# Performance work log

Hardware: AMD Instinct MI355X
Metric: run time of the kernel (lower is better)

## Reference

```python
import jax, jax.numpy as jnp
from jax import lax
import numpy as np

B, OBS, PRED, F, H = 2048, 20, 30, 16, 1024


def _lstm_layer(x, Wih, Whh, bih, bhh):
    # x: [T, B, in]; PyTorch gate order i, f, g, o; zero initial state
    Bb = x.shape[1]
    Hh = Whh.shape[1]
    def step(carry, xt):
        h, c = carry
        g = xt @ Wih.T + h @ Whh.T + bih + bhh
        i, f, gg, o = jnp.split(g, 4, axis=-1)
        c = jax.nn.sigmoid(f) * c + jax.nn.sigmoid(i) * jnp.tanh(gg)
        h = jax.nn.sigmoid(o) * jnp.tanh(c)
        return (h, c), h
    z = jnp.zeros((Bb, Hh), x.dtype)
    _, hs = lax.scan(step, (z, z), x)
    return hs  # [T, B, H]


def _lstm2(x, Wih0, Whh0, bih0, bhh0, Wih1, Whh1, bih1, bhh1):
    return _lstm_layer(_lstm_layer(x, Wih0, Whh0, bih0, bhh0), Wih1, Whh1, bih1, bhh1)


def setup_inputs() -> dict:
    key = jax.random.key(0)
    ks = jax.random.split(key, 32)
    s = 0.05
    def w(k, shape):
        return jax.random.normal(k, shape, dtype=jnp.float32) * s
    d = {
        'x_in': jax.random.normal(ks[0], (B, OBS, F), dtype=jnp.float32),
        'y': jax.random.normal(ks[1], (B, PRED, F), dtype=jnp.float32),
        'v_in': jax.random.normal(ks[2], (B, OBS, F), dtype=jnp.float32),
        'sx': jnp.ones((1,), jnp.float32),
        'sv': jnp.ones((1,), jnp.float32),
    }
    i = 3
    for p in ['v', 'a']:
        d[p + 'Wih0'] = w(ks[i], (4 * H, F)); i += 1
        d[p + 'Whh0'] = w(ks[i], (4 * H, H)); i += 1
        d[p + 'bih0'] = w(ks[i], (4 * H,)); i += 1
        d[p + 'bhh0'] = w(ks[i], (4 * H,)); i += 1
        d[p + 'Wih1'] = w(ks[i], (4 * H, H)); i += 1
        d[p + 'Whh1'] = w(ks[i], (4 * H, H)); i += 1
        d[p + 'bih1'] = w(ks[i], (4 * H,)); i += 1
        d[p + 'bhh1'] = w(ks[i], (4 * H,)); i += 1
        d[p + 'Wl'] = w(ks[i], (F, H)); i += 1
        d[p + 'bl'] = w(ks[i], (F,)); i += 1
    return d


def reference(x_in, y, v_in, sx, sv,
              vWih0, vWhh0, vbih0, vbhh0, vWih1, vWhh1, vbih1, vbhh1, vWl, vbl,
              aWih0, aWhh0, abih0, abhh0, aWih1, aWhh1, abih1, abhh1, aWl, abl):
    # last observed position, scaled: [1, B, F]
    x = jnp.transpose(x_in, (1, 0, 2))[-1:] * sx
    yT = sx * jnp.transpose(y, (1, 0, 2))  # [PRED, B, F]
    v_seq = jnp.transpose(v_in, (1, 0, 2))  # [OBS, B, F]
    a_seq = v_seq[1:] - v_seq[:-1]          # [OBS-1, B, F]

    vh = _lstm2(v_seq, vWih0, vWhh0, vbih0, vbhh0, vWih1, vWhh1, vbih1, vbhh1)
    v = sv * jnp.tanh(vh[-1:] @ vWl.T + vbl)  # [1, B, F]

    ah = _lstm2(a_seq, aWih0, aWhh0, abih0, abhh0, aWih1, aWhh1, abih1, abhh1)
    a = jnp.tanh(ah @ aWl.T + abl)[-1:]       # [1, B, F] (unscaled, fed back)

    v = v + sv * a
    x = x + v

    def body(carry, _):
        a, v, x = carry
        # NOTE: faithful to source -- LSTM state resets to zero each step
        ah = _lstm2(a, aWih0, aWhh0, abih0, abhh0, aWih1, aWhh1, abih1, abhh1)
        a = jnp.tanh(ah @ aWl.T + abl)
        v = v + sv * a
        x = x + v
        return (a, v, x), x[0]

    _, xs = lax.scan(body, (a, v, x), None, length=PRED - 1)  # xs: [PRED-1, B, F]
    out = jnp.concatenate([x, xs], axis=0)  # [PRED, B, F]
    return (out, yT)
```

## Files before the change

kernel.cpp:

```cpp
#include <hip/hip_runtime.h>


#define B_    2048
#define OBS_  20
#define PRED_ 30
#define F_    16
#define H_    1024
#define GN_   4096

typedef _Float16 f16;
typedef _Float16 f16x8 __attribute__((ext_vector_type(8)));
typedef _Float16 f16x4 __attribute__((ext_vector_type(4)));
typedef float    f32x4 __attribute__((ext_vector_type(4)));

__device__ __forceinline__ float fast_sigmoid(float x) {
  return 1.0f / (1.0f + __expf(-x));
}
__device__ __forceinline__ float fast_tanh(float x) {
  float ax = fabsf(x);
  float e  = __expf(-2.0f * ax);
  float r  = (1.0f - e) / (1.0f + e);
  return copysignf(r, x);
}

__device__ __forceinline__ void stageA(f16* dst, const f16* Asrc, int b0, int k0, int tid) {
#pragma unroll
  for (int cc = 0; cc < 2; ++cc) {
    int o  = cc * 4096 + tid * 16;
    int rr = o >> 6;
    int sp = (o >> 4) & 3;
    int sl = sp ^ ((rr >> 1) & 3);
    const f16* gp = Asrc + (size_t)(b0 + rr) * H_ + k0 + sl * 8;
    __builtin_amdgcn_global_load_lds(
        (const __attribute__((address_space(1))) void*)gp,
        (__attribute__((address_space(3))) void*)((char*)dst + o), 16, 0, 0);
  }
}
__device__ __forceinline__ void stageB(f16* dst, const f16* Wsrc, int j0, int k0, int tid) {
#pragma unroll
  for (int cc = 0; cc < 2; ++cc) {
    int o  = cc * 4096 + tid * 16;
    int rr = o >> 6;
    int sp = (o >> 4) & 3;
    int sl = sp ^ ((rr >> 1) & 3);
    int row = (rr >> 5) * H_ + j0 + (rr & 31);
    const f16* gp = Wsrc + (size_t)row * H_ + k0 + sl * 8;
    __builtin_amdgcn_global_load_lds(
        (const __attribute__((address_space(1))) void*)gp,
        (__attribute__((address_space(3))) void*)((char*)dst + o), 16, 0, 0);
  }
}

__device__ __forceinline__ void acc_init(f32x4 (&acc)[4][4], const float* bias, int jcol) {
#pragma unroll
  for (int g = 0; g < 4; ++g) {
    float bv = bias[g * H_ + jcol];
#pragma unroll
    for (int m = 0; m < 4; ++m) acc[m][g] = (f32x4){bv, bv, bv, bv};
  }
}

__device__ __forceinline__ void run_k16(f32x4 (&acc)[4][4], const f16* A16, const f16* W16,
    int b0, int j0, int wr, int wc, int lcol, int lkq)
{
  f16x8 za = {0, 0, 0, 0, 0, 0, 0, 0};
  f16x8 af[4], bf[4];
#pragma unroll
  for (int m = 0; m < 4; ++m) {
    if (lkq < 2) {
      int row = b0 + wr * 64 + m * 16 + lcol;
      af[m] = *(const f16x8*)(A16 + (size_t)row * 16 + lkq * 8);
    } else af[m] = za;
  }
#pragma unroll
  for (int g = 0; g < 4; ++g) {
    if (lkq < 2) {
      int row = g * H_ + j0 + wc * 16 + lcol;
      bf[g] = *(const f16x8*)(W16 + (size_t)row * 16 + lkq * 8);
    } else bf[g] = za;
  }
#pragma unroll
  for (int m = 0; m < 4; ++m)
#pragma unroll
    for (int g = 0; g < 4; ++g)
      acc[m][g] = __builtin_amdgcn_mfma_f32_16x16x32_f16(af[m], bf[g], acc[m][g], 0, 0, 0);
}

__device__ __forceinline__ void kstep_mfma(f32x4 (&acc)[4][4], const f16* lA, const f16* lB,
    int wr, int wc, int lcol, int lkq)
{
  f16x8 av[4], bw[4];
#pragma unroll
  for (int m = 0; m < 4; ++m) {
    int ar = wr * 64 + m * 16 + lcol;
    int sa = lkq ^ ((ar >> 1) & 3);
    av[m] = *(const f16x8*)&lA[ar * 32 + sa * 8];
  }
#pragma unroll
  for (int g = 0; g < 4; ++g) {
    int br = g * 32 + wc * 16 + lcol;
    int sb = lkq ^ ((br >> 1) & 3);
    bw[g] = *(const f16x8*)&lB[br * 32 + sb * 8];
  }
#pragma unroll
  for (int m = 0; m < 4; ++m)
#pragma unroll
    for (int g = 0; g < 4; ++g)
      acc[m][g] = __builtin_amdgcn_mfma_f32_16x16x32_f16(av[m], bw[g], acc[m][g], 0, 0, 0);
}

__device__ __forceinline__ void run_kloop_rt(f32x4 (&acc)[4][4],
    f16 (*lA)[4096], f16 (*lB)[4096],
    const f16* A0, const f16* W0, const f16* A1, const f16* W1,
    int NT, int NTSW,
    int b0, int j0, int tid, int wr, int wc, int lcol, int lkq)
{
  int cur = 0;
  for (int t = 0; t < NT; ++t) {
    if (t + 1 < NT) {
      int tn = t + 1;
      const f16* As = (tn >= NTSW) ? A1 : A0;
      const f16* Ws = (tn >= NTSW) ? W1 : W0;
      int k0 = (tn & 31) * 32;
      stageA(lA[cur ^ 1], As, b0, k0, tid);
      stageB(lB[cur ^ 1], Ws, j0, k0, tid);
      asm volatile("s_waitcnt vmcnt(4)\n\ts_barrier" ::: "memory");
    } else {
      asm volatile("s_waitcnt vmcnt(0)\n\ts_barrier" ::: "memory");
    }
    kstep_mfma(acc, lA[cur], lB[cur], wr, wc, lcol, lkq);
    asm volatile("s_waitcnt lgkmcnt(0)\n\ts_barrier" ::: "memory");
    cur ^= 1;
  }
}

__device__ __forceinline__ void lstm_epi_g(f32x4 (&acc)[4][4], const float* cin, float* cout,
    f16* hout, int b0, int jcol, int wr, int lkq, int hasc, int writec)
{
#pragma unroll
  for (int m = 0; m < 4; ++m) {
    int brow0 = b0 + wr * 64 + m * 16 + lkq * 4;
#pragma unroll
    for (int r = 0; r < 4; ++r) {
      size_t bi = (size_t)(brow0 + r) * H_ + jcol;
      float gi = acc[m][0][r], gf = acc[m][1][r], gg = acc[m][2][r], go = acc[m][3][r];
      float cold = hasc ? cin[bi] : 0.0f;
      float cn = fast_sigmoid(gf) * cold + fast_sigmoid(gi) * fast_tanh(gg);
      float hv = fast_sigmoid(go) * fast_tanh(cn);
      if (writec) cout[bi] = cn;
      hout[bi] = (f16)hv;
    }
  }
}

struct StepArgs {
  const f16* A16; const f16* W16v; const f16* W16a;
  const f16* A0;  const f16* W0v;  const f16* W0a;
  const f16* A1;  const f16* W1v;  const f16* W1a;
  const float* bv; const float* ba;
  const float* cin; float* cout; f16* hout;
  int k16, nt, hasc, writec;
};

__device__ __forceinline__ void lstm_body(const StepArgs& p, f16 (*lA)[4096], f16 (*lB)[4096], int bi)
{
  const int tid = threadIdx.x, lane = tid & 63;
  const int wv = tid >> 6, wr = wv >> 1, wc = wv & 1;
  const int bm = bi >> 5, bn = bi & 31;
  const int b0 = bm * 128, j0 = bn * 32;
  const int ch = bm >> 4;
  const int lcol = lane & 15, lkq = lane >> 4;
  const int jcol = j0 + wc * 16 + lcol;

  const f16* W16 = ch ? p.W16a : p.W16v;
  const f16* W0  = ch ? p.W0a  : p.W0v;
  const f16* W1  = ch ? p.W1a  : p.W1v;
  const float* bias = ch ? p.ba : p.bv;

  if (p.nt) { stageA(lA[0], p.A0, b0, 0, tid); stageB(lB[0], W0, j0, 0, tid); }
  f32x4 acc[4][4];
  acc_init(acc, bias, jcol);
  if (p.k16) run_k16(acc, p.A16, W16, b0, j0, wr, wc, lcol, lkq);
  if (p.nt)
    run_kloop_rt(acc, lA, lB, p.A0, W0, p.A1, W1, p.nt, 32, b0, j0, tid, wr, wc, lcol, lkq);
  lstm_epi_g(acc, p.cin, p.cout, p.hout, b0, jcol, wr, lkq, p.hasc, p.writec);
}

__global__ __launch_bounds__(256, 4)
void obs_pair(StepArgs q, StepArgs r, int split)
{
  __shared__ f16 lA[2][4096];
  __shared__ f16 lB[2][4096];
  int blk = blockIdx.x;
  if (blk < split) lstm_body(q, lA, lB, blk);
  else             lstm_body(r, lA, lB, blk - split);
}

__global__ __launch_bounds__(256, 4)
void scan_l1(const f16* __restrict__ h0, const f16* __restrict__ Wih1,
             const float* __restrict__ bias1, const float* __restrict__ Wl,
             float* __restrict__ ppart)
{
  __shared__ f16 lA[2][4096];
  __shared__ f16 lB[2][4096];
  __shared__ f16 hl[128 * 40];
  const int tid = threadIdx.x, lane = tid & 63;
  const int wv = tid >> 6, wr = wv >> 1, wc = wv & 1;
  const int bm = blockIdx.x >> 5, bn = blockIdx.x & 31;
  const int b0 = bm * 128, j0 = bn * 32;
  const int lcol = lane & 15, lkq = lane >> 4;
  const int jcol = j0 + wc * 16 + lcol;

  stageA(lA[0], h0, b0, 0, tid);
  stageB(lB[0], Wih1, j0, 0, tid);
  f32x4 acc[4][4];
  acc_init(acc, bias1, jcol);
  run_kloop_rt(acc, lA, lB, h0, Wih1, nullptr, nullptr, 32, 32, b0, j0, tid, wr, wc, lcol, lkq);

  int jl = wc * 16 + lcol;
#pragma unroll
  for (int m = 0; m < 4; ++m) {
#pragma unroll
    for (int r = 0; r < 4; ++r) {
      int row = wr * 64 + m * 16 + lkq * 4 + r;
      float gi = acc[m][0][r], gf = acc[m][1][r], gg = acc[m][2][r], go = acc[m][3][r];
      (void)gf;
      float cn = fast_sigmoid(gi) * fast_tanh(gg);
      float hv = fast_sigmoid(go) * fast_tanh(cn);
      hl[row * 40 + jl] = (f16)hv;
    }
  }
  __syncthreads();

  const float* wrow = Wl + (size_t)lcol * H_ + j0 + lkq * 8;
  float4 w0 = *(const float4*)wrow, w1 = *(const float4*)(wrow + 4);
  f16x8 bf = {(f16)w0.x, (f16)w0.y, (f16)w0.z, (f16)w0.w,
              (f16)w1.x, (f16)w1.y, (f16)w1.z, (f16)w1.w};
#pragma unroll
  for (int mt = 0; mt < 2; ++mt) {
    int arow = wv * 32 + mt * 16 + lcol;
    f16x8 af = *(const f16x8*)&hl[arow * 40 + lkq * 8];
    f32x4 pc = {0, 0, 0, 0};
    pc = __builtin_amdgcn_mfma_f32_16x16x32_f16(af, bf, pc, 0, 0, 0);
#pragma unroll
    for (int r = 0; r < 4; ++r) {
      int row = b0 + wv * 32 + mt * 16 + lkq * 4 + r;
      ppart[(size_t)row * 512 + bn * 16 + lcol] = pc[r];
    }
  }
}

template<int FIRST, int LAST>
__global__ __launch_bounds__(256, 4)
void scan_l0(const float* __restrict__ ppart, const f16* __restrict__ a16f,
             const float* __restrict__ bl, const float* __restrict__ sv,
             float* __restrict__ v_buf, float* __restrict__ x_buf,
             float* __restrict__ out_t,
             const float* __restrict__ bias0, const f16* __restrict__ Wih0,
             f16* __restrict__ h0out)
{
  __shared__ f16 a_lds[128 * 16];
  const int tid = threadIdx.x;
  const int bm = LAST ? (int)blockIdx.x : (int)(blockIdx.x >> 5);
  const int bn = LAST ? 0 : (int)(blockIdx.x & 31);
  const int b0 = bm * 128;

  const int ebase = tid * 8;
  const int erow  = ebase >> 4;
  const int ef0   = ebase & 15;
  float av[8];
  if (FIRST) {
    f16x8 a8 = *(const f16x8*)&a16f[(size_t)(b0 + erow) * 16 + ef0];
#pragma unroll
    for (int e = 0; e < 8; ++e) av[e] = (float)a8[e];
  } else {
    f32x4 s0 = {0, 0, 0, 0}, s1 = {0, 0, 0, 0};
    const float* pp = ppart + (size_t)(b0 + erow) * 512 + ef0;
#pragma unroll
    for (int sN = 0; sN < 32; ++sN) {
      s0 += *(const f32x4*)(pp + sN * 16);
      s1 += *(const f32x4*)(pp + sN * 16 + 4);
    }
#pragma unroll
    for (int e = 0; e < 4; ++e) av[e] = fast_tanh(s0[e] + bl[ef0 + e]);
#pragma unroll
    for (int e = 0; e < 4; ++e) av[4 + e] = fast_tanh(s1[e] + bl[ef0 + 4 + e]);
    if (bn == 0) {
      float svv = sv[0];
#pragma unroll
      for (int e = 0; e < 8; ++e) {
        int idx = (b0 + erow) * F_ + ef0 + e;
        float v = v_buf[idx] + svv * av[e];
        v_buf[idx] = v;
        float x = x_buf[idx] + v;
        x_buf[idx] = x;
        out_t[idx] = x;
      }
    }
  }

  if (!LAST) {
    f16x8 a8;
#pragma unroll
    for (int e = 0; e < 8; ++e) a8[e] = (f16)av[e];
    *(f16x8*)&a_lds[ebase] = a8;
    __syncthreads();

    const int lane = tid & 63;
    const int wv = tid >> 6, wr = wv >> 1, wc = wv & 1;
    const int lcol = lane & 15, lkq = lane >> 4;
    const int j0 = bn * 32, jcol = j0 + wc * 16 + lcol;
    f32x4 acc[4][4];
    acc_init(acc, bias0, jcol);
    f16x8 za = {0, 0, 0, 0, 0, 0, 0, 0};
    f16x8 af[4], bf[4];
#pragma unroll
    for (int m = 0; m < 4; ++m) {
      if (lkq < 2) {
        int arow = wr * 64 + m * 16 + lcol;
        af[m] = *(const f16x8*)&a_lds[arow * 16 + lkq * 8];
      } else af[m] = za;
    }
#pragma unroll
    for (int g = 0; g < 4; ++g) {
      if (lkq < 2) {
        int brow = g * H_ + j0 + wc * 16 + lcol;
        bf[g] = *(const f16x8*)(Wih0 + (size_t)brow * 16 + lkq * 8);
      } else bf[g] = za;
    }
#pragma unroll
    for (int m = 0; m < 4; ++m)
#pragma unroll
      for (int g = 0; g < 4; ++g)
        acc[m][g] = __builtin_amdgcn_mfma_f32_16x16x32_f16(af[m], bf[g], acc[m][g], 0, 0, 0);
    lstm_epi_g(acc, nullptr, nullptr, h0out, b0, jcol, wr, lkq, 0, 0);
  }
}

template<int MODE>
__global__ __launch_bounds__(256)
void proj_update(const f16* __restrict__ h1, const float* __restrict__ Wl,
                 const float* __restrict__ bl, const float* __restrict__ sv,
                 float* __restrict__ v_buf, float* __restrict__ x_buf,
                 float* __restrict__ out_t, f16* __restrict__ a16)
{
  __shared__ f16 lh[16 * 1024];
  const int b0r = blockIdx.x * 16;
  const int tid = threadIdx.x;
#pragma unroll
  for (int c = 0; c < 8; ++c) {
    int o = c * 256 + tid;
    *(f16x8*)&lh[o * 8] = *(const f16x8*)&h1[(size_t)b0r * 1024 + o * 8];
  }
  __syncthreads();
  const int br = tid >> 4;
  const int f  = tid & 15;
  float s0 = 0, s1 = 0, s2 = 0, s3 = 0;
  const float4* wp = (const float4*)(Wl + (size_t)f * 1024);
#pragma unroll 4
  for (int k8 = 0; k8 < 128; ++k8) {
    f16x8 hv = *(const f16x8*)&lh[br * 1024 + k8 * 8];
    float4 w0 = wp[k8 * 2], w1 = wp[k8 * 2 + 1];
    s0 += (float)hv[0] * w0.x + (float)hv[4] * w1.x;
    s1 += (float)hv[1] * w0.y + (float)hv[5] * w1.y;
    s2 += (float)hv[2] * w0.z + (float)hv[6] * w1.z;
    s3 += (float)hv[3] * w0.w + (float)hv[7] * w1.w;
  }
  float t = fast_tanh(bl[f] + ((s0 + s1) + (s2 + s3)));
  int idx = (b0r + br) * F_ + f;
  if (MODE == 0) {
    v_buf[idx] = sv[0] * t;
  } else {
    float v = v_buf[idx] + sv[0] * t;
    v_buf[idx] = v;
    float x = x_buf[idx] + v;
    x_buf[idx] = x;
    out_t[idx] = x;
    a16[idx] = (f16)t;
  }
}

__global__ void prep_kernel(const float* __restrict__ x_in, const float* __restrict__ y,
                            const float* __restrict__ v_in, const float* __restrict__ sx,
                            float* __restrict__ out, float* __restrict__ x_buf,
                            f16* __restrict__ m16)
{
  const float s = sx[0];
  int gid = blockIdx.x * blockDim.x + threadIdx.x;
  int gs  = gridDim.x * blockDim.x;
  for (int i = gid; i < B_ * OBS_ * F_; i += gs) {
    int b = i / (OBS_ * F_);
    int rem = i - b * (OBS_ * F_);
    int t = rem >> 4;
    int f = rem & 15;
    float v = v_in[i];
    m16[((size_t)t * 4096 + b) * F_ + f] = (f16)v;
    if (t < OBS_ - 1)
      m16[((size_t)t * 4096 + 2048 + b) * F_ + f] = (f16)(v_in[i + F_] - v);
  }
  for (int i = gid; i < PRED_ * B_ * F_; i += gs) {
    int t = i / (B_ * F_);
    int rem = i - t * (B_ * F_);
    int b = rem >> 4;
    int f = rem & 15;
    out[PRED_ * B_ * F_ + i] = s * y[(b * PRED_ + t) * F_ + f];
  }
  for (int i = gid; i < B_ * F_; i += gs) {
    int b = i >> 4;
    int f = i & 15;
    x_buf[i] = s * x_in[(b * OBS_ + (OBS_ - 1)) * F_ + f];
  }
}

struct ConvArgs {
  const float* src[8];
  f16*         dst[8];
  int          n[8];
  const float* b1[4];
  const float* b2[4];
  float*       bd[4];
};

__global__ void convw(ConvArgs a)
{
  int gid = blockIdx.x * blockDim.x + threadIdx.x;
  int gs  = gridDim.x * blockDim.x;
#pragma unroll
  for (int s = 0; s < 8; ++s) {
    int n4 = a.n[s] >> 2;
    for (int i = gid; i < n4; i += gs) {
      float4 v = ((const float4*)a.src[s])[i];
      f16x4 d = {(f16)v.x, (f16)v.y, (f16)v.z, (f16)v.w};
      ((f16x4*)a.dst[s])[i] = d;
    }
  }
#pragma unroll
  for (int s = 0; s < 4; ++s) {
    for (int i = gid; i < GN_; i += gs) a.bd[s][i] = a.b1[s][i] + a.b2[s][i];
  }
}

extern "C" void kernel_launch(void* const* d_in, const int* in_sizes, int n_in,
                              void* d_out, int out_size, void* d_ws, size_t ws_size,
                              hipStream_t stream)
{
  (void)in_sizes; (void)n_in; (void)out_size; (void)ws_size;

  const float* x_in  = (const float*)d_in[0];
  const float* y     = (const float*)d_in[1];
  const float* v_in  = (const float*)d_in[2];
  const float* sx    = (const float*)d_in[3];
  const float* sv    = (const float*)d_in[4];
  const float* vWih0 = (const float*)d_in[5];
  const float* vWhh0 = (const float*)d_in[6];
  const float* vbih0 = (const float*)d_in[7];
  const float* vbhh0 = (const float*)d_in[8];
  const float* vWih1 = (const float*)d_in[9];
  const float* vWhh1 = (const float*)d_in[10];
  const float* vbih1 = (const float*)d_in[11];
  const float* vbhh1 = (const float*)d_in[12];
  const float* vWl   = (const float*)d_in[13];
  const float* vbl   = (const float*)d_in[14];
  const float* aWih0 = (const float*)d_in[15];
  const float* aWhh0 = (const float*)d_in[16];
  const float* abih0 = (const float*)d_in[17];
  const float* abhh0 = (const float*)d_in[18];
  const float* aWih1 = (const float*)d_in[19];
  const float* aWhh1 = (const float*)d_in[20];
  const float* abih1 = (const float*)d_in[21];
  const float* abhh1 = (const float*)d_in[22];
  const float* aWl   = (const float*)d_in[23];
  const float* abl   = (const float*)d_in[24];
  float* out = (float*)d_out;

  char* ws = (char*)d_ws;
  size_t off = 0;
  auto alloc = [&](size_t bytes) {
    char* p = ws + off;
    off += (bytes + 255) & ~(size_t)255;
    return p;
  };
  f16* vWih0f = (f16*)alloc((size_t)GN_ * F_ * 2);
  f16* vWhh0f = (f16*)alloc((size_t)GN_ * H_ * 2);
  f16* vWih1f = (f16*)alloc((size_t)GN_ * H_ * 2);
  f16* vWhh1f = (f16*)alloc((size_t)GN_ * H_ * 2);
  f16* aWih0f = (f16*)alloc((size_t)GN_ * F_ * 2);
  f16* aWhh0f = (f16*)alloc((size_t)GN_ * H_ * 2);
  f16* aWih1f = (f16*)alloc((size_t)GN_ * H_ * 2);
  f16* aWhh1f = (f16*)alloc((size_t)GN_ * H_ * 2);
  float* vb0 = (float*)alloc(GN_ * 4);
  float* vb1 = (float*)alloc(GN_ * 4);
  float* ab0 = (float*)alloc(GN_ * 4);
  float* ab1 = (float*)alloc(GN_ * 4);
  f16* m16 = (f16*)alloc((size_t)OBS_ * 4096 * F_ * 2);
  f16* h0a = (f16*)alloc((size_t)4096 * H_ * 2);
  f16* h0b = (f16*)alloc((size_t)4096 * H_ * 2);
  f16* h1a = (f16*)alloc((size_t)4096 * H_ * 2);
  f16* h1b = (f16*)alloc((size_t)4096 * H_ * 2);
  float* c0 = (float*)alloc((size_t)4096 * H_ * 4);
  float* c1 = (float*)alloc((size_t)4096 * H_ * 4);
  f16* a16   = (f16*)alloc((size_t)B_ * F_ * 2);
  float* v_buf = (float*)alloc((size_t)B_ * F_ * 4);
  float* x_buf = (float*)alloc((size_t)B_ * F_ * 4);
  float* ppart = (float*)alloc((size_t)B_ * 32 * F_ * 4);

  ConvArgs ca;
  ca.src[0] = vWih0; ca.dst[0] = vWih0f; ca.n[0] = GN_ * F_;
  ca.src[1] = vWhh0; ca.dst[1] = vWhh0f; ca.n[1] = GN_ * H_;
  ca.src[2] = vWih1; ca.dst[2] = vWih1f; ca.n[2] = GN_ * H_;
  ca.src[3] = vWhh1; ca.dst[3] = vWhh1f; ca.n[3] = GN_ * H_;
  ca.src[4] = aWih0; ca.dst[4] = aWih0f; ca.n[4] = GN_ * F_;
  ca.src[5] = aWhh0; ca.dst[5] = aWhh0f; ca.n[5] = GN_ * H_;
  ca.src[6] = aWih1; ca.dst[6] = aWih1f; ca.n[6] = GN_ * H_;
  ca.src[7] = aWhh1; ca.dst[7] = aWhh1f; ca.n[7] = GN_ * H_;
  ca.b1[0] = vbih0; ca.b2[0] = vbhh0; ca.bd[0] = vb0;
  ca.b1[1] = vbih1; ca.b2[1] = vbhh1; ca.bd[1] = vb1;
  ca.b1[2] = abih0; ca.b2[2] = abhh0; ca.bd[2] = ab0;
  ca.b1[3] = abih1; ca.b2[3] = abhh1; ca.bd[3] = ab1;
  convw<<<1024, 256, 0, stream>>>(ca);
  prep_kernel<<<1024, 256, 0, stream>>>(x_in, y, v_in, sx, out, x_buf, m16);

  auto h0buf = [&](int t) { return (t & 1) ? h0b : h0a; };
  auto h1buf = [&](int t) { return (t & 1) ? h1b : h1a; };
  StepArgs dummy{};

  {
    StepArgs q{};
    q.A16 = m16; q.W16v = vWih0f; q.W16a = aWih0f;
    q.bv = vb0; q.ba = ab0;
    q.cout = c0; q.hout = h0buf(0);
    q.k16 = 1; q.nt = 0; q.hasc = 0; q.writec = 1;
    obs_pair<<<1024, 256, 0, stream>>>(q, dummy, 1024);
  }

  for (int t = 1; t < OBS_; ++t) {
    int u = t - 1;
    StepArgs q{};
    q.A16 = m16 + (size_t)t * 4096 * F_;
    q.W16v = vWih0f; q.W16a = aWih0f;
    q.A0 = h0buf(t - 1); q.W0v = vWhh0f; q.W0a = aWhh0f;
    q.bv = vb0; q.ba = ab0;
    q.cin = c0; q.cout = c0; q.hout = h0buf(t);
    q.k16 = 1; q.nt = 32; q.hasc = 1; q.writec = 1;

    StepArgs r{};
    r.A0 = h0buf(u); r.W0v = vWih1f; r.W0a = aWih1f;
    r.A1 = (u > 0) ? h1buf(u - 1) : nullptr;
    r.W1v = vWhh1f; r.W1a = aWhh1f;
    r.bv = vb1; r.ba = ab1;
    r.cin = c1; r.cout = c1; r.hout = h1buf(u);
    r.k16 = 0; r.nt = (u > 0) ? 64 : 32; r.hasc = (u > 0); r.writec = 1;

    int split = (t == OBS_ - 1) ? 512 : 1024;
    int grid  = (t == OBS_ - 1) ? 1536 : 2048;
    obs_pair<<<grid, 256, 0, stream>>>(q, r, split);
  }

  {
    StepArgs r{};
    r.A0 = h0buf(19); r.W0v = vWih1f; r.W0a = aWih1f;
    r.A1 = h1buf(18); r.W1v = vWhh1f; r.W1a = aWhh1f;
    r.bv = vb1; r.ba = ab1;
    r.cin = c1; r.cout = c1; r.hout = h1buf(19);
    r.k16 = 0; r.nt = 64; r.hasc = 1; r.writec = 1;
    obs_pair<<<512, 256, 0, stream>>>(dummy, r, 0);
  }

  proj_update<0><<<128, 256, 0, stream>>>(h1buf(19), vWl, vbl, sv,
                                          v_buf, nullptr, nullptr, nullptr);
  proj_update<1><<<128, 256, 0, stream>>>(h1buf(18) + (size_t)2048 * H_, aWl, abl, sv,
                                          v_buf, x_buf, out, a16);

  scan_l0<1, 0><<<512, 256, 0, stream>>>(ppart, a16, abl, sv, v_buf, x_buf, out,
                                         ab0, aWih0f, h0a);
  scan_l1<<<512, 256, 0, stream>>>(h0a, aWih1f, ab1, aWl, ppart);
  for (int t = 2; t < PRED_; ++t) {
    scan_l0<0, 0><<<512, 256, 0, stream>>>(ppart, nullptr, abl, sv, v_buf, x_buf,
                                           out + (size_t)(t - 1) * B_ * F_,
                                           ab0, aWih0f, h0a);
    scan_l1<<<512, 256, 0, stream>>>(h0a, aWih1f, ab1, aWl, ppart);
  }
  scan_l0<0, 1><<<16, 256, 0, stream>>>(ppart, nullptr, abl, sv, v_buf, x_buf,
                                        out + (size_t)(PRED_ - 1) * B_ * F_,
                                        ab0, aWih0f, h0a);
}
```

Before: 4.395 ms.

## Widen LSTM GEMM tiles to 128x64 hidden columns with 512-thread blocks

Each block now covers 64 hidden units (256 gate columns) instead of 32 and runs 8 waves in a 2x4 arrangement, which halves the grid and the number of times each A tile of h is re-read across blocks. The staging helpers, LDS B buffer, swizzle row indexing, the projection epilogue in scan_l1 and the ppart partial-sum width (32 to 16 partials) are all adjusted to match. The long layer-1 work is also placed first in the split grid so it is scheduled before the short layer-0 blocks. The trade-off is fewer blocks, which risks lower occupancy and poorer load balance on a GPU with many CUs, plus more LDS per block.

```diff
diff --git a/kernel.cpp b/kernel.cpp
--- a/kernel.cpp
+++ b/kernel.cpp
@@ -23,28 +23,25 @@
   return copysignf(r, x);
 }
 
-__device__ __forceinline__ void stageA(f16* dst, const f16* Asrc, int b0, int k0, int tid) {
+__device__ __forceinline__ void stageA512(f16* dst, const f16* Asrc, int b0, int k0, int tid) {
+  int o  = tid * 16;
+  int rr = o >> 6;
+  int sp = (o >> 4) & 3;
+  int sl = sp ^ ((rr >> 1) & 3);
+  const f16* gp = Asrc + (size_t)(b0 + rr) * H_ + k0 + sl * 8;
+  __builtin_amdgcn_global_load_lds(
+      (const __attribute__((address_space(1))) void*)gp,
+      (__attribute__((address_space(3))) void*)((char*)dst + o), 16, 0, 0);
+}
+__device__ __forceinline__ void stageB512(f16* dst, const f16* Wsrc, int j0, int k0, int tid) {
 #pragma unroll
   for (int cc = 0; cc < 2; ++cc) {
-    int o  = cc * 4096 + tid * 16;
+    int o  = cc * 8192 + tid * 16;
     int rr = o >> 6;
     int sp = (o >> 4) & 3;
     int sl = sp ^ ((rr >> 1) & 3);
-    const f16* gp = Asrc + (size_t)(b0 + rr) * H_ + k0 + sl * 8;
-    __builtin_amdgcn_global_load_lds(
-        (const __attribute__((address_space(1))) void*)gp,
-        (__attribute__((address_space(3))) void*)((char*)dst + o), 16, 0, 0);
-  }
-}
-__device__ __forceinline__ void stageB(f16* dst, const f16* Wsrc, int j0, int k0, int tid) {
-#pragma unroll
-  for (int cc = 0; cc < 2; ++cc) {
-    int o  = cc * 4096 + tid * 16;
-    int rr = o >> 6;
-    int sp = (o >> 4) & 3;
-    int sl = sp ^ ((rr >> 1) & 3);
-    int row = (rr >> 5) * H_ + j0 + (rr & 31);
-    const f16* gp = Wsrc + (size_t)row * H_ + k0 + sl * 8;
+    int grow = (rr >> 6) * H_ + j0 + (rr & 63);
+    const f16* gp = Wsrc + (size_t)grow * H_ + k0 + sl * 8;
     __builtin_amdgcn_global_load_lds(
         (const __attribute__((address_space(1))) void*)gp,
         (__attribute__((address_space(3))) void*)((char*)dst + o), 16, 0, 0);
@@ -98,7 +95,7 @@
   }
 #pragma unroll
   for (int g = 0; g < 4; ++g) {
-    int br = g * 32 + wc * 16 + lcol;
+    int br = g * 64 + wc * 16 + lcol;
     int sb = lkq ^ ((br >> 1) & 3);
     bw[g] = *(const f16x8*)&lB[br * 32 + sb * 8];
   }
@@ -109,8 +106,8 @@
       acc[m][g] = __builtin_amdgcn_mfma_f32_16x16x32_f16(av[m], bw[g], acc[m][g], 0, 0, 0);
 }
 
-__device__ __forceinline__ void run_kloop_rt(f32x4 (&acc)[4][4],
-    f16 (*lA)[4096], f16 (*lB)[4096],
+__device__ __forceinline__ void run_kloop(f32x4 (&acc)[4][4],
+    f16 (*lA)[4096], f16 (*lB)[8192],
     const f16* A0, const f16* W0, const f16* A1, const f16* W1,
     int NT, int NTSW,
     int b0, int j0, int tid, int wr, int wc, int lcol, int lkq)
@@ -122,9 +119,9 @@
       const f16* As = (tn >= NTSW) ? A1 : A0;
       const f16* Ws = (tn >= NTSW) ? W1 : W0;
       int k0 = (tn & 31) * 32;
-      stageA(lA[cur ^ 1], As, b0, k0, tid);
-      stageB(lB[cur ^ 1], Ws, j0, k0, tid);
-      asm volatile("s_waitcnt vmcnt(4)\n\ts_barrier" ::: "memory");
+      stageA512(lA[cur ^ 1], As, b0, k0, tid);
+      stageB512(lB[cur ^ 1], Ws, j0, k0, tid);
+      asm volatile("s_waitcnt vmcnt(3)\n\ts_barrier" ::: "memory");
     } else {
       asm volatile("s_waitcnt vmcnt(0)\n\ts_barrier" ::: "memory");
     }
@@ -162,12 +159,13 @@
   int k16, nt, hasc, writec;
 };
 
-__device__ __forceinline__ void lstm_body(const StepArgs& p, f16 (*lA)[4096], f16 (*lB)[4096], int bi)
+__device__ __forceinline__ void lstm_body(const StepArgs& p, f16 (*lA)[4096], f16 (*lB)[8192], int bi)
 {
   const int tid = threadIdx.x, lane = tid & 63;
-  const int wv = tid >> 6, wr = wv >> 1, wc = wv & 1;
-  const int bm = bi >> 5, bn = bi & 31;
-  const int b0 = bm * 128, j0 = bn * 32;
+  const int wv = tid >> 6;
+  const int wr = wv >> 2, wc = wv & 3;
+  const int bm = bi >> 4, bn = bi & 15;
+  const int b0 = bm * 128, j0 = bn * 64;
   const int ch = bm >> 4;
   const int lcol = lane & 15, lkq = lane >> 4;
   const int jcol = j0 + wc * 16 + lcol;
@@ -177,45 +175,46 @@
   const f16* W1  = ch ? p.W1a  : p.W1v;
   const float* bias = ch ? p.ba : p.bv;
 
-  if (p.nt) { stageA(lA[0], p.A0, b0, 0, tid); stageB(lB[0], W0, j0, 0, tid); }
+  if (p.nt) { stageA512(lA[0], p.A0, b0, 0, tid); stageB512(lB[0], W0, j0, 0, tid); }
   f32x4 acc[4][4];
   acc_init(acc, bias, jcol);
   if (p.k16) run_k16(acc, p.A16, W16, b0, j0, wr, wc, lcol, lkq);
   if (p.nt)
-    run_kloop_rt(acc, lA, lB, p.A0, W0, p.A1, W1, p.nt, 32, b0, j0, tid, wr, wc, lcol, lkq);
+    run_kloop(acc, lA, lB, p.A0, W0, p.A1, W1, p.nt, 32, b0, j0, tid, wr, wc, lcol, lkq);
   lstm_epi_g(acc, p.cin, p.cout, p.hout, b0, jcol, wr, lkq, p.hasc, p.writec);
 }
 
-__global__ __launch_bounds__(256, 4)
-void obs_pair(StepArgs q, StepArgs r, int split)
+__global__ __launch_bounds__(512, 4)
+void obs_pair(StepArgs rlong, StepArgs qshort, int split)
 {
   __shared__ f16 lA[2][4096];
-  __shared__ f16 lB[2][4096];
+  __shared__ f16 lB[2][8192];
   int blk = blockIdx.x;
-  if (blk < split) lstm_body(q, lA, lB, blk);
-  else             lstm_body(r, lA, lB, blk - split);
-}
-
-__global__ __launch_bounds__(256, 4)
+  if (blk < split) lstm_body(rlong, lA, lB, blk);
+  else             lstm_body(qshort, lA, lB, blk - split);
+}
+
+__global__ __launch_bounds__(512, 2)
 void scan_l1(const f16* __restrict__ h0, const f16* __restrict__ Wih1,
              const float* __restrict__ bias1, const float* __restrict__ Wl,
              float* __restrict__ ppart)
 {
   __shared__ f16 lA[2][4096];
-  __shared__ f16 lB[2][4096];
-  __shared__ f16 hl[128 * 40];
+  __shared__ f16 lB[2][8192];
+  __shared__ f16 hl[128 * 72];
   const int tid = threadIdx.x, lane = tid & 63;
-  const int wv = tid >> 6, wr = wv >> 1, wc = wv & 1;
-  const int bm = blockIdx.x >> 5, bn = blockIdx.x & 31;
-  const int b0 = bm * 128, j0 = bn * 32;
+  const int wv = tid >> 6;
+  const int wr = wv >> 2, wc = wv & 3;
+  const int bm = blockIdx.x >> 4, bn = blockIdx.x & 15;
+  const int b0 = bm * 128, j0 = bn * 64;
   const int lcol = lane & 15, lkq = lane >> 4;
   const int jcol = j0 + wc * 16 + lcol;
 
-  stageA(lA[0], h0, b0, 0, tid);
-  stageB(lB[0], Wih1, j0, 0, tid);
+  stageA512(lA[0], h0, b0, 0, tid);
+  stageB512(lB[0], Wih1, j0, 0, tid);
   f32x4 acc[4][4];
   acc_init(acc, bias1, jcol);
-  run_kloop_rt(acc, lA, lB, h0, Wih1, nullptr, nullptr, 32, 32, b0, j0, tid, wr, wc, lcol, lkq);
+  run_kloop(acc, lA, lB, h0, Wih1, nullptr, nullptr, 32, 32, b0, j0, tid, wr, wc, lcol, lkq);
 
   int jl = wc * 16 + lcol;
 #pragma unroll
@@ -223,30 +222,28 @@
 #pragma unroll
     for (int r = 0; r < 4; ++r) {
       int row = wr * 64 + m * 16 + lkq * 4 + r;
-      float gi = acc[m][0][r], gf = acc[m][1][r], gg = acc[m][2][r], go = acc[m][3][r];
-      (void)gf;
+      float gi = acc[m][0][r], gg = acc[m][2][r], go = acc[m][3][r];
       float cn = fast_sigmoid(gi) * fast_tanh(gg);
       float hv = fast_sigmoid(go) * fast_tanh(cn);
-      hl[row * 40 + jl] = (f16)hv;
+      hl[row * 72 + jl] = (f16)hv;
     }
   }
   __syncthreads();
 
-  const float* wrow = Wl + (size_t)lcol * H_ + j0 + lkq * 8;
-  float4 w0 = *(const float4*)wrow, w1 = *(const float4*)(wrow + 4);
-  f16x8 bf = {(f16)w0.x, (f16)w0.y, (f16)w0.z, (f16)w0.w,
-              (f16)w1.x, (f16)w1.y, (f16)w1.z, (f16)w1.w};
-#pragma unroll
-  for (int mt = 0; mt < 2; ++mt) {
-    int arow = wv * 32 + mt * 16 + lcol;
-    f16x8 af = *(const f16x8*)&hl[arow * 40 + lkq * 8];
-    f32x4 pc = {0, 0, 0, 0};
-    pc = __builtin_amdgcn_mfma_f32_16x16x32_f16(af, bf, pc, 0, 0, 0);
-#pragma unroll
-    for (int r = 0; r < 4; ++r) {
-      int row = b0 + wv * 32 + mt * 16 + lkq * 4 + r;
-      ppart[(size_t)row * 512 + bn * 16 + lcol] = pc[r];
-    }
+  const float* wp = Wl + (size_t)lcol * H_ + j0 + lkq * 8;
+  f16x8 bf0, bf1;
+#pragma unroll
+  for (int e = 0; e < 8; ++e) { bf0[e] = (f16)wp[e]; bf1[e] = (f16)wp[32 + e]; }
+  int arow = wv * 16 + lcol;
+  f16x8 af0 = *(const f16x8*)&hl[arow * 72 + lkq * 8];
+  f16x8 af1 = *(const f16x8*)&hl[arow * 72 + 32 + lkq * 8];
+  f32x4 pc = {0, 0, 0, 0};
+  pc = __builtin_amdgcn_mfma_f32_16x16x32_f16(af0, bf0, pc, 0, 0, 0);
+  pc = __builtin_amdgcn_mfma_f32_16x16x32_f16(af1, bf1, pc, 0, 0, 0);
+#pragma unroll
+  for (int r = 0; r < 4; ++r) {
+    int prow = b0 + wv * 16 + lkq * 4 + r;
+    ppart[(size_t)prow * 256 + bn * 16 + lcol] = pc[r];
   }
 }
 
@@ -275,9 +272,9 @@
     for (int e = 0; e < 8; ++e) av[e] = (float)a8[e];
   } else {
     f32x4 s0 = {0, 0, 0, 0}, s1 = {0, 0, 0, 0};
-    const float* pp = ppart + (size_t)(b0 + erow) * 512 + ef0;
-#pragma unroll
-    for (int sN = 0; sN < 32; ++sN) {
+    const float* pp = ppart + (size_t)(b0 + erow) * 256 + ef0;
+#pragma unroll
+    for (int sN = 0; sN < 16; ++sN) {
       s0 += *(const f32x4*)(pp + sN * 16);
       s1 += *(const f32x4*)(pp + sN * 16 + 4);
     }
@@ -502,7 +499,7 @@
   f16* a16   = (f16*)alloc((size_t)B_ * F_ * 2);
   float* v_buf = (float*)alloc((size_t)B_ * F_ * 4);
   float* x_buf = (float*)alloc((size_t)B_ * F_ * 4);
-  float* ppart = (float*)alloc((size_t)B_ * 32 * F_ * 4);
+  float* ppart = (float*)alloc((size_t)B_ * 16 * F_ * 4);
 
   ConvArgs ca;
   ca.src[0] = vWih0; ca.dst[0] = vWih0f; ca.n[0] = GN_ * F_;
@@ -530,7 +527,7 @@
     q.bv = vb0; q.ba = ab0;
     q.cout = c0; q.hout = h0buf(0);
     q.k16 = 1; q.nt = 0; q.hasc = 0; q.writec = 1;
-    obs_pair<<<1024, 256, 0, stream>>>(q, dummy, 1024);
+    obs_pair<<<512, 512, 0, stream>>>(dummy, q, 0);
   }
 
   for (int t = 1; t < OBS_; ++t) {
@@ -551,9 +548,8 @@
     r.cin = c1; r.cout = c1; r.hout = h1buf(u);
     r.k16 = 0; r.nt = (u > 0) ? 64 : 32; r.hasc = (u > 0); r.writec = 1;
 
-    int split = (t == OBS_ - 1) ? 512 : 1024;
-    int grid  = (t == OBS_ - 1) ? 1536 : 2048;
-    obs_pair<<<grid, 256, 0, stream>>>(q, r, split);
+    int qblocks = (t == OBS_ - 1) ? 256 : 512;
+    obs_pair<<<512 + qblocks, 512, 0, stream>>>(r, q, 512);
   }
 
   {
@@ -563,7 +559,7 @@
     r.bv = vb1; r.ba = ab1;
     r.cin = c1; r.cout = c1; r.hout = h1buf(19);
     r.k16 = 0; r.nt = 64; r.hasc = 1; r.writec = 1;
-    obs_pair<<<512, 256, 0, stream>>>(dummy, r, 0);
+    obs_pair<<<256, 512, 0, stream>>>(r, dummy, 256);
   }
 
   proj_update<0><<<128, 256, 0, stream>>>(h1buf(19), vWl, vbl, sv,
@@ -573,12 +569,12 @@
 
   scan_l0<1, 0><<<512, 256, 0, stream>>>(ppart, a16, abl, sv, v_buf, x_buf, out,
                                          ab0, aWih0f, h0a);
-  scan_l1<<<512, 256, 0, stream>>>(h0a, aWih1f, ab1, aWl, ppart);
+  scan_l1<<<256, 512, 0, stream>>>(h0a, aWih1f, ab1, aWl, ppart);
   for (int t = 2; t < PRED_; ++t) {
     scan_l0<0, 0><<<512, 256, 0, stream>>>(ppart, nullptr, abl, sv, v_buf, x_buf,
                                            out + (size_t)(t - 1) * B_ * F_,
                                            ab0, aWih0f, h0a);
-    scan_l1<<<512, 256, 0, stream>>>(h0a, aWih1f, ab1, aWl, ppart);
+    scan_l1<<<256, 512, 0, stream>>>(h0a, aWih1f, ab1, aWl, ppart);
   }
   scan_l0<0, 1><<<16, 256, 0, stream>>>(ppart, nullptr, abl, sv, v_buf, x_buf,
                                         out + (size_t)(PRED_ - 1) * B_ * F_,
```

After: 4.204 ms. 4.3% less time.
